# Kernel tuning notes

Hardware: AMD Instinct MI355X
Metric: run time of the kernel (lower is better)

The kernel has to match this reference:

```python
import jax, jax.numpy as jnp
import numpy as np

B, S, D = 4, 2048, 1024

def setup_inputs() -> dict:
    key = jax.random.key(0)
    k1, k2, k3, k4 = jax.random.split(key, 4)
    scale = 1.0 / np.sqrt(D)
    x = jax.random.normal(k1, (B, S, D), dtype=jnp.float32)
    Wq = jax.random.normal(k2, (D, D), dtype=jnp.float32) * scale
    Wk = jax.random.normal(k3, (D, D), dtype=jnp.float32) * scale
    Wv = jax.random.normal(k4, (D, D), dtype=jnp.float32) * scale
    return {"x": x, "Wq": Wq, "Wk": Wk, "Wv": Wv}

def reference(x, Wq, Wk, Wv):
    # Linear projections (nn.Linear with bias=False computes x @ W.T)
    q = jnp.einsum('bsd,ed->bse', x, Wq)
    k = jnp.einsum('bsd,ed->bse', x, Wk)
    v = jnp.einsum('bsd,ed->bse', x, Wv)
    # HRR binding: circular convolution of k and v == elementwise product in FFT domain
    fq = jnp.fft.fft(q, axis=-1)
    fk = jnp.fft.fft(k, axis=-1)
    fv = jnp.fft.fft(v, axis=-1)
    # Causal associative memory: cumulative sum of bound key-value pairs over sequence
    mem = jnp.cumsum(fk * fv, axis=-2)  # [B, S, D] complex
    # Unbind with query via approximate inverse (complex conjugate of fft(q))
    out = jnp.fft.ifft(mem * jnp.conj(fq), axis=-1).real
    return out.astype(x.dtype)
```

## Files before the change

kernel.cpp:

```cpp
#include <hip/hip_runtime.h>

#define BB 4
#define SS 2048
#define DD 1024
#define MM 8192
#define CH 64
#define RR 32
#define PI_F 3.14159265358979323846f

typedef __attribute__((ext_vector_type(8))) short bf16x8;
typedef __attribute__((ext_vector_type(4))) float f32x4;

__device__ __forceinline__ unsigned short f2bf(float f) {
  unsigned int u = __float_as_uint(f);
  u = (u + 0x7FFFu + ((u >> 16) & 1u)) >> 16;
  return (unsigned short)u;
}
__device__ __forceinline__ float bf2f(unsigned short h) {
  return __uint_as_float(((unsigned int)h) << 16);
}

__global__ __launch_bounds__(256) void convert_bf16(
    const float* __restrict__ src, unsigned short* __restrict__ dst) {
  const long i = ((long)blockIdx.x * 256 + threadIdx.x) * 4;
  const float4 v = *(const float4*)&src[i];
  ushort4 o;
  o.x = f2bf(v.x); o.y = f2bf(v.y); o.z = f2bf(v.z); o.w = f2bf(v.w);
  *(ushort4*)&dst[i] = o;
}

__global__ __launch_bounds__(256) void convert_w(
    const float* __restrict__ Wq, const float* __restrict__ Wk,
    const float* __restrict__ Wv, unsigned short* __restrict__ dst) {
  const int z = blockIdx.y;
  const float* src = (z == 0) ? Wq : (z == 1) ? Wk : Wv;
  const long i = ((long)blockIdx.x * 256 + threadIdx.x) * 4;
  const float4 v = *(const float4*)&src[i];
  ushort4 o;
  o.x = f2bf(v.x); o.y = f2bf(v.y); o.z = f2bf(v.z); o.w = f2bf(v.w);
  *(ushort4*)&dst[(size_t)z * DD * DD + i] = o;
}

__device__ __forceinline__ void async16(const void* g, void* l) {
  __builtin_amdgcn_global_load_lds(
      (const __attribute__((address_space(1))) void*)g,
      (__attribute__((address_space(3))) void*)l, 16, 0, 0);
}

#define GW(n)  asm volatile("s_waitcnt vmcnt(" #n ")" ::: "memory")
#define BAR()  asm volatile("s_barrier" ::: "memory")
#define SB0()  __builtin_amdgcn_sched_barrier(0)

#define STA(buf, i, T) async16(xb + (size_t)(m0 + 64 * (i)) * DD + (T) * 64 + aOff, \
                               &Als[(buf) * 16384 + (i) * 4096 + slot8])
#define STB(buf, p, T) async16(W + (size_t)(n0 + 16 * (p)) * DD + (T) * 64 + bOff, \
                               &Bls[(buf) * 16384 + (p) * 4096 + slot8])
#define LDA(buf) { _Pragma("unroll") for (int mt = 0; mt < 8; ++mt) { \
    af[mt][0] = *(const bf16x8*)&Als[(buf) * 16384 + aRd + mt * 1024 + qoff0]; \
    af[mt][1] = *(const bf16x8*)&Als[(buf) * 16384 + aRd + mt * 1024 + qoff1]; } }
#define LDB(buf, p, bank) { \
    bank[0] = *(const bf16x8*)&Bls[(buf) * 16384 + (p) * 4096 + bRd + qoff0]; \
    bank[1] = *(const bf16x8*)&Bls[(buf) * 16384 + (p) * 4096 + bRd + qoff1]; }
#define MMA(p, bank) { __builtin_amdgcn_s_setprio(1); \
    _Pragma("unroll") for (int mt = 0; mt < 8; ++mt) { \
      acc[mt][p] = __builtin_amdgcn_mfma_f32_16x16x32_bf16(af[mt][0], bank[0], acc[mt][p], 0, 0, 0); \
      acc[mt][p] = __builtin_amdgcn_mfma_f32_16x16x32_bf16(af[mt][1], bank[1], acc[mt][p], 0, 0, 0); } \
    __builtin_amdgcn_s_setprio(0); }

__global__ __launch_bounds__(512, 2) void gemm_mfma(
    const unsigned short* __restrict__ xb,
    const unsigned short* __restrict__ Wb,
    float* __restrict__ outq, unsigned short* __restrict__ KV) {
  const int z = blockIdx.z;
  const unsigned short* W = Wb + (size_t)z * DD * DD;

  __shared__ unsigned short Als[2 * 16384];
  __shared__ unsigned short Bls[2 * 16384];

  const int tid  = threadIdx.x;
  const int lane = tid & 63;
  const int w    = tid >> 6;
  const int wm   = w >> 2;
  const int gq   = w & 3;
  const int fr   = lane & 15;
  const int kq   = lane >> 4;

  const int m0 = blockIdx.x * 256;
  const int n0 = blockIdx.y * 256;

  const int slot  = tid;
  const int srow  = slot >> 3;
  const int sq    = (slot & 7) ^ (srow & 7);
  const int slot8 = slot * 8;
  const size_t aOff = (size_t)srow * DD + sq * 8;
  const size_t bOff = (size_t)(64 * (slot >> 7) + ((slot >> 3) & 15)) * DD + sq * 8;

  const int qoff0 = ((0 + kq) ^ (fr & 7)) * 8;
  const int qoff1 = ((4 + kq) ^ (fr & 7)) * 8;
  const int aRd = wm * 8192 + fr * 64;
  const int bRd = gq * 1024 + fr * 64;

  f32x4 acc[8][4] = {};
  bf16x8 af[8][2];
  bf16x8 bva[2], bvb[2];

  STA(0, 0, 0); STA(0, 1, 0);
  STA(0, 2, 0); STB(0, 0, 0);
  STA(0, 3, 0); STB(0, 1, 0);
  STB(0, 2, 0); STB(0, 3, 0);
  STA(1, 0, 1); STA(1, 1, 1);
  STA(1, 2, 1); STB(1, 0, 1);
  STA(1, 3, 1); STB(1, 1, 1);

  for (int T = 0; T < 14; ++T) {
    const int buf = T & 1;
    SB0(); GW(6); BAR();
    LDA(buf); LDB(buf, 0, bva);
    STB(buf ^ 1, 2, T + 1); STB(buf ^ 1, 3, T + 1);
    LDB(buf, 1, bvb);
    MMA(0, bva);
    SB0(); BAR();
    STA(buf, 0, T + 2); STA(buf, 1, T + 2);
    LDB(buf, 2, bva);
    MMA(1, bvb);
    SB0(); BAR();
    STA(buf, 2, T + 2); STB(buf, 0, T + 2);
    LDB(buf, 3, bvb);
    MMA(2, bva);
    SB0(); BAR();
    STA(buf, 3, T + 2); STB(buf, 1, T + 2);
    MMA(3, bvb);
  }
  SB0(); GW(6); BAR();
  LDA(0); LDB(0, 0, bva);
  STB(1, 2, 15); STB(1, 3, 15);
  LDB(0, 1, bvb);
  MMA(0, bva);
  SB0(); BAR(); LDB(0, 2, bva); MMA(1, bvb);
  SB0(); BAR(); LDB(0, 3, bvb); MMA(2, bva);
  SB0(); BAR(); MMA(3, bvb);
  SB0(); GW(0); BAR();
  LDA(1); LDB(1, 0, bva); LDB(1, 1, bvb);
  MMA(0, bva);
  SB0(); BAR(); LDB(1, 2, bva); MMA(1, bvb);
  SB0(); BAR(); LDB(1, 3, bvb); MMA(2, bva);
  SB0(); BAR(); MMA(3, bvb);

  const int col = lane & 15;
  const int r0  = (lane >> 4) * 4;
  const int mBase = m0 + wm * 128;
  const int nBase = n0 + gq * 64;
  if (z == 0) {
    #pragma unroll
    for (int mt = 0; mt < 8; ++mt)
      #pragma unroll
      for (int p = 0; p < 4; ++p)
        #pragma unroll
        for (int r = 0; r < 4; ++r)
          outq[(size_t)(mBase + mt * 16 + r0 + r) * DD + nBase + p * 16 + col] =
              acc[mt][p][r];
  } else {
    unsigned short* Ck = KV + (size_t)(z - 1) * DD;
    #pragma unroll
    for (int mt = 0; mt < 8; ++mt)
      #pragma unroll
      for (int p = 0; p < 4; ++p)
        #pragma unroll
        for (int r = 0; r < 4; ++r)
          Ck[(size_t)(mBase + mt * 16 + r0 + r) * 2048 + nBase + p * 16 + col] =
              f2bf(acc[mt][p][r]);
  }
}

__device__ __forceinline__ int pidx(int i) { return i + (i >> 6); }
#define BUFSZ 1040
__device__ __forceinline__ int pidx16(int i) { return i + (i >> 4); }
#define MEMSZ 546

__device__ __forceinline__ int rev4(int p) {
  unsigned r = __brev((unsigned)p) >> 22;
  return (int)(((r & 0x155u) << 1) | ((r & 0x2AAu) >> 1));
}

__host__ __device__ constexpr int clog2(int s) {
  return (s == 256) ? 8 : (s == 64) ? 6 : (s == 16) ? 4 : (s == 4) ? 2 : 0;
}

template <int S>
__device__ __forceinline__ void fwd_stage(float2 x[4], int t) {
  float c1 = 1.0f, s1 = 0.0f;
  if (S > 1) {
    const int j = t & (S - 1);
    __sincosf(-2.0f * PI_F * (float)j / (float)(4 * S), &s1, &c1);
  }
  const float c2 = c1 * c1 - s1 * s1, s2 = 2.0f * c1 * s1;
  const float c3 = c1 * c2 - s1 * s2, s3 = c1 * s2 + s1 * c2;
  const float Ar = x[0].x + x[2].x, Ai = x[0].y + x[2].y;
  const float Br = x[1].x + x[3].x, Bi = x[1].y + x[3].y;
  const float Cr = x[0].x - x[2].x, Ci = x[0].y - x[2].y;
  const float dr = x[1].x - x[3].x, di = x[1].y - x[3].y;
  const float y1r = Cr + di, y1i = Ci - dr;
  const float y2r = Ar - Br, y2i = Ai - Bi;
  const float y3r = Cr - di, y3i = Ci + dr;
  x[0] = make_float2(Ar + Br, Ai + Bi);
  x[1] = make_float2(y1r * c1 - y1i * s1, y1r * s1 + y1i * c1);
  x[2] = make_float2(y2r * c2 - y2i * s2, y2r * s2 + y2i * c2);
  x[3] = make_float2(y3r * c3 - y3i * s3, y3r * s3 + y3i * c3);
}

template <int S>
__device__ __forceinline__ void inv_stage(float2 x[4], int t) {
  float c1 = 1.0f, s1 = 0.0f;
  if (S > 1) {
    const int j = t & (S - 1);
    __sincosf(2.0f * PI_F * (float)j / (float)(4 * S), &s1, &c1);
  }
  const float c2 = c1 * c1 - s1 * s1, s2 = 2.0f * c1 * s1;
  const float c3 = c1 * c2 - s1 * s2, s3 = c1 * s2 + s1 * c2;
  const float u0r = x[0].x,                   u0i = x[0].y;
  const float u1r = x[1].x * c1 - x[1].y * s1, u1i = x[1].x * s1 + x[1].y * c1;
  const float u2r = x[2].x * c2 - x[2].y * s2, u2i = x[2].x * s2 + x[2].y * c2;
  const float u3r = x[3].x * c3 - x[3].y * s3, u3i = x[3].x * s3 + x[3].y * c3;
  const float Er = u0r + u2r, Ei = u0i + u2i;
  const float Fr = u0r - u2r, Fi = u0i - u2i;
  const float Gr = u1r + u3r, Gi = u1i + u3i;
  const float Hr = u1r - u3r, Hi = u1i - u3i;
  x[0] = make_float2(Er + Gr, Ei + Gi);
  x[1] = make_float2(Fr - Hi, Fi + Hr);
  x[2] = make_float2(Er - Gr, Ei - Gi);
  x[3] = make_float2(Fr + Hi, Fi - Hr);
}

template <int SW, int SR>
__device__ __forceinline__ void xchg(float2* buf, float2 x[4], int t) {
  constexpr int LW2 = clog2(SW), LR = clog2(SR);
  #pragma unroll
  for (int n = 0; n < 4; ++n)
    buf[pidx(((t >> LW2) << (LW2 + 2)) + (t & (SW - 1)) + n * SW)] = x[n];
  __syncthreads();
  #pragma unroll
  for (int n = 0; n < 4; ++n)
    x[n] = buf[pidx(((t >> LR) << (LR + 2)) + (t & (SR - 1)) + n * SR)];
  __syncthreads();
}

__device__ __forceinline__ void fwd_fft(float2* buf, float2 x[4], int t) {
  fwd_stage<256>(x, t); xchg<256, 64>(buf, x, t);
  fwd_stage<64>(x, t);  xchg<64, 16>(buf, x, t);
  fwd_stage<16>(x, t);  xchg<16, 4>(buf, x, t);
  fwd_stage<4>(x, t);   xchg<4, 1>(buf, x, t);
  fwd_stage<1>(x, t);
  #pragma unroll
  for (int n = 0; n < 4; ++n) buf[pidx(4 * t + n)] = x[n];
  __syncthreads();
}

__global__ __launch_bounds__(256) void bind_kernel(unsigned short* __restrict__ KV) {
  __shared__ float2 buf[BUFSZ];
  const int t = threadIdx.x;
  unsigned short* row = KV + (long)blockIdx.x * 2048;

  float2 x[4];
  #pragma unroll
  for (int n = 0; n < 4; ++n) {
    const int i = t + 256 * n;
    x[n] = make_float2(bf2f(row[i]), bf2f(row[1024 + i]));
  }
  fwd_fft(buf, x, t);

  float2* Prow = (float2*)row;
  #pragma unroll
  for (int m = 0; m < 2; ++m) {
    const int s = t + 256 * m;
    if (s == 0) {
      const float2 W0   = buf[pidx(0)];
      const float2 W512 = buf[pidx(2)];
      Prow[0] = make_float2(W0.x * W0.y, W512.x * W512.y);
    } else {
      const int p1 = rev4(s);
      const int p2 = rev4(1024 - s);
      const float2 F1 = buf[pidx(p1)], F2 = buf[pidx(p2)];
      const float fkr = 0.5f * (F1.x + F2.x), fki = 0.5f * (F1.y - F2.y);
      const float fvr = 0.5f * (F1.y + F2.y), fvi = 0.5f * (F2.x - F1.x);
      Prow[s] = make_float2(fkr * fvr - fki * fvi, fkr * fvi + fki * fvr);
    }
  }
}

__global__ __launch_bounds__(256) void scan_chunk_sum(
    const float2* __restrict__ P, float2* __restrict__ csum) {
  const int chunk = blockIdx.x;
  const int batch = blockIdx.y >> 1;
  const int f = (blockIdx.y & 1) * 256 + threadIdx.x;
  long base = ((long)batch * SS + (long)chunk * RR) * 512 + f;
  float sr = 0.0f, si = 0.0f;
  #pragma unroll
  for (int i0 = 0; i0 < RR; i0 += 8) {
    float2 p[8];
    #pragma unroll
    for (int j = 0; j < 8; ++j) p[j] = P[base + (long)(i0 + j) * 512];
    #pragma unroll
    for (int j = 0; j < 8; ++j) { sr += p[j].x; si += p[j].y; }
  }
  csum[((long)batch * CH + chunk) * 512 + f] = make_float2(sr, si);
}

__global__ __launch_bounds__(256) void scan_chunk_scan(float2* csum) {
  const int idx = blockIdx.x * 256 + threadIdx.x;
  const int batch = idx >> 9;
  const int f = idx & 511;
  float2 v[CH];
  #pragma unroll
  for (int c = 0; c < CH; ++c) v[c] = csum[((long)batch * CH + c) * 512 + f];
  float rr = 0.0f, ri = 0.0f;
  #pragma unroll
  for (int c = 0; c < CH; ++c) {
    const float2 x = v[c];
    csum[((long)batch * CH + c) * 512 + f] = make_float2(rr, ri);
    rr += x.x; ri += x.y;
  }
}

__global__ __launch_bounds__(256) void scan_apply(
    float2* __restrict__ P, const float2* __restrict__ csum) {
  const int chunk = blockIdx.x;
  const int batch = blockIdx.y >> 1;
  const int f = (blockIdx.y & 1) * 256 + threadIdx.x;
  float2 off = csum[((long)batch * CH + chunk) * 512 + f];
  float ar = off.x, ai = off.y;
  long base = ((long)batch * SS + (long)chunk * RR) * 512 + f;
  #pragma unroll
  for (int i0 = 0; i0 < RR; i0 += 8) {
    float2 p[8];
    #pragma unroll
    for (int j = 0; j < 8; ++j) p[j] = P[base + (long)(i0 + j) * 512];
    #pragma unroll
    for (int j = 0; j < 8; ++j) {
      ar += p[j].x; ai += p[j].y;
      P[base + (long)(i0 + j) * 512] = make_float2(ar, ai);
    }
  }
}

__global__ __launch_bounds__(256) void unbind_kernel(
    float* __restrict__ qout, const float2* __restrict__ mem) {
  __shared__ float2 buf[BUFSZ];
  __shared__ float2 m0s[MEMSZ], m1s[MEMSZ];
  const int t = threadIdx.x;
  const long r0 = (long)blockIdx.x * 2;
  float* row0 = qout + r0 * DD;
  float* row1 = row0 + DD;
  const float2* mem0 = mem + r0 * 512;
  const float2* mem1 = mem0 + 512;

  float2 x[4];
  #pragma unroll
  for (int n = 0; n < 4; ++n) {
    const int i = t + 256 * n;
    x[n] = make_float2(row0[i], row1[i]);
  }
  #pragma unroll
  for (int n = 0; n < 2; ++n) {
    const int s = t + 256 * n;
    const float2 a = mem0[s], b = mem1[s];
    if (s == 0) {
      m0s[pidx16(0)]   = make_float2(a.x, 0.0f);
      m0s[pidx16(512)] = make_float2(a.y, 0.0f);
      m1s[pidx16(0)]   = make_float2(b.x, 0.0f);
      m1s[pidx16(512)] = make_float2(b.y, 0.0f);
    } else {
      m0s[pidx16(s)] = a;
      m1s[pidx16(s)] = b;
    }
  }
  fwd_fft(buf, x, t);

  float2 z[4];
  #pragma unroll
  for (int m = 0; m < 4; ++m) {
    const int p   = t + 256 * m;
    const int bin = rev4(p);
    const int p2  = rev4((1024 - bin) & 1023);
    const float2 F1 = buf[pidx(p)], F2 = buf[pidx(p2)];
    const float q0r = 0.5f * (F1.x + F2.x), q0i = 0.5f * (F1.y - F2.y);
    const float q1r = 0.5f * (F1.y + F2.y), q1i = 0.5f * (F2.x - F1.x);
    const int  ix = (bin <= 512) ? bin : 1024 - bin;
    const float sg = (bin <= 512) ? 1.0f : -1.0f;
    float2 m0 = m0s[pidx16(ix)], m1 = m1s[pidx16(ix)];
    m0.y *= sg; m1.y *= sg;
    const float z0r = m0.x * q0r + m0.y * q0i, z0i = m0.y * q0r - m0.x * q0i;
    const float z1r = m1.x * q1r + m1.y * q1i, z1i = m1.y * q1r - m1.x * q1i;
    z[m] = make_float2(z0r - z1i, z0i + z1r);
  }
  __syncthreads();
  #pragma unroll
  for (int m = 0; m < 4; ++m) buf[pidx(t + 256 * m)] = z[m];
  __syncthreads();
  #pragma unroll
  for (int n = 0; n < 4; ++n) x[n] = buf[pidx(4 * t + n)];

  inv_stage<1>(x, t);   xchg<1, 4>(buf, x, t);
  inv_stage<4>(x, t);   xchg<4, 16>(buf, x, t);
  inv_stage<16>(x, t);  xchg<16, 64>(buf, x, t);
  inv_stage<64>(x, t);  xchg<64, 256>(buf, x, t);
  inv_stage<256>(x, t);

  const float sc = 1.0f / 1024.0f;
  #pragma unroll
  for (int n = 0; n < 4; ++n) {
    const int i = t + 256 * n;
    row0[i] = x[n].x * sc;
    row1[i] = x[n].y * sc;
  }
}

extern "C" void kernel_launch(void* const* d_in, const int* in_sizes, int n_in,
                              void* d_out, int out_size, void* d_ws, size_t ws_size,
                              hipStream_t stream) {
  (void)in_sizes; (void)n_in; (void)out_size;
  const float* x  = (const float*)d_in[0];
  const float* Wq = (const float*)d_in[1];
  const float* Wk = (const float*)d_in[2];
  const float* Wv = (const float*)d_in[3];
  float* out = (float*)d_out;

  const size_t wbytes = (size_t)3 * DD * DD * 2;
  auto need = [&](size_t MHr, size_t nB) {
    return wbytes + MHr * DD * 2 + MHr * 4096 + nB * CH * 512 * 8;
  };
  const int nPass = (ws_size >= need(8192, 4)) ? 1 : 2;
  const size_t MH = MM / nPass;
  const int    nB = BB / nPass;

  char* ws = (char*)d_ws;
  unsigned short* Wb = (unsigned short*)ws;
  unsigned short* xb = (unsigned short*)(ws + wbytes);
  unsigned short* KV = (unsigned short*)(ws + wbytes + MH * DD * 2);
  float2*       csum = (float2*)((char*)KV + MH * 4096);

  convert_w<<<dim3(DD * DD / 1024, 3), 256, 0, stream>>>(Wq, Wk, Wv, Wb);

  for (int h = 0; h < nPass; ++h) {
    const float* xh   = x   + (size_t)h * MH * DD;
    float*       outh = out + (size_t)h * MH * DD;

    convert_bf16<<<MH * DD / 1024, 256, 0, stream>>>(xh, xb);
    gemm_mfma<<<dim3(MH / 256, DD / 256, 3), dim3(512), 0, stream>>>(xb, Wb, outh, KV);
    bind_kernel<<<MH, 256, 0, stream>>>(KV);
    scan_chunk_sum<<<dim3(CH, nB * 2), 256, 0, stream>>>((const float2*)KV, csum);
    scan_chunk_scan<<<nB * 2, 256, 0, stream>>>(csum);
    scan_apply<<<dim3(CH, nB * 2), 256, 0, stream>>>((float2*)KV, csum);
    unbind_kernel<<<MH / 2, 256, 0, stream>>>(outh, (const float2*)KV);
  }
}
```

Baseline: 233.5 us.

## Restructure GEMM main loop to two barriers per K-tile with grouped LDS stores

Reorganizes the software-pipelined projection GEMM loop so each K-tile uses two barrier phases instead of four, grouping the global-to-LDS stores for the next stages together and issuing two MFMA groups per phase. The prologue issues stage loads in a different order and the vmcnt wait threshold drops from 6 to 4. This is meant to cut barrier and synchronisation overhead and give the MFMA stream longer uninterrupted runs. In exchange it changes how closely loads overlap compute and raises the risk of LDS hazards if any buffer reuse ordering is wrong.

```diff
diff --git a/kernel.cpp b/kernel.cpp
--- a/kernel.cpp
+++ b/kernel.cpp
@@ -104,47 +104,41 @@
   bf16x8 af[8][2];
   bf16x8 bva[2], bvb[2];
 
-  STA(0, 0, 0); STA(0, 1, 0);
-  STA(0, 2, 0); STB(0, 0, 0);
-  STA(0, 3, 0); STB(0, 1, 0);
-  STB(0, 2, 0); STB(0, 3, 0);
-  STA(1, 0, 1); STA(1, 1, 1);
-  STA(1, 2, 1); STB(1, 0, 1);
-  STA(1, 3, 1); STB(1, 1, 1);
+  STA(0, 0, 0); STA(0, 1, 0); STA(0, 2, 0); STA(0, 3, 0);
+  STB(0, 0, 0); STB(0, 1, 0); STB(0, 2, 0); STB(0, 3, 0);
+  STA(1, 0, 1); STA(1, 1, 1); STB(1, 0, 1); STB(1, 1, 1);
 
   for (int T = 0; T < 14; ++T) {
     const int buf = T & 1;
-    SB0(); GW(6); BAR();
-    LDA(buf); LDB(buf, 0, bva);
+    SB0(); GW(4); BAR();
+    LDB(buf, 0, bva);
+    LDA(buf);
+    LDB(buf, 1, bvb);
     STB(buf ^ 1, 2, T + 1); STB(buf ^ 1, 3, T + 1);
-    LDB(buf, 1, bvb);
+    STA(buf ^ 1, 2, T + 1); STA(buf ^ 1, 3, T + 1);
     MMA(0, bva);
-    SB0(); BAR();
-    STA(buf, 0, T + 2); STA(buf, 1, T + 2);
-    LDB(buf, 2, bva);
     MMA(1, bvb);
     SB0(); BAR();
-    STA(buf, 2, T + 2); STB(buf, 0, T + 2);
+    LDB(buf, 2, bva);
     LDB(buf, 3, bvb);
+    STA(buf, 0, T + 2); STA(buf, 1, T + 2);
+    STB(buf, 0, T + 2); STB(buf, 1, T + 2);
     MMA(2, bva);
-    SB0(); BAR();
-    STA(buf, 3, T + 2); STB(buf, 1, T + 2);
     MMA(3, bvb);
   }
-  SB0(); GW(6); BAR();
-  LDA(0); LDB(0, 0, bva);
-  STB(1, 2, 15); STB(1, 3, 15);
-  LDB(0, 1, bvb);
-  MMA(0, bva);
-  SB0(); BAR(); LDB(0, 2, bva); MMA(1, bvb);
-  SB0(); BAR(); LDB(0, 3, bvb); MMA(2, bva);
-  SB0(); BAR(); MMA(3, bvb);
+  SB0(); GW(4); BAR();
+  LDB(0, 0, bva); LDA(0); LDB(0, 1, bvb);
+  STB(1, 2, 15); STB(1, 3, 15); STA(1, 2, 15); STA(1, 3, 15);
+  MMA(0, bva); MMA(1, bvb);
+  SB0(); BAR();
+  LDB(0, 2, bva); LDB(0, 3, bvb);
+  MMA(2, bva); MMA(3, bvb);
   SB0(); GW(0); BAR();
-  LDA(1); LDB(1, 0, bva); LDB(1, 1, bvb);
-  MMA(0, bva);
-  SB0(); BAR(); LDB(1, 2, bva); MMA(1, bvb);
-  SB0(); BAR(); LDB(1, 3, bvb); MMA(2, bva);
-  SB0(); BAR(); MMA(3, bvb);
+  LDB(1, 0, bva); LDA(1); LDB(1, 1, bvb);
+  MMA(0, bva); MMA(1, bvb);
+  SB0(); BAR();
+  LDB(1, 2, bva); LDB(1, 3, bvb);
+  MMA(2, bva); MMA(3, bvb);
 
   const int col = lane & 15;
   const int r0  = (lane >> 4) * 4;
```

New measurement: 228.7 us. 1.02x faster.
